# Kernel tuning notes

Measured on AMD Instinct MI355X. Metric: run time of the kernel, lower is better.

Reference implementation:

```python
import jax, jax.numpy as jnp
import numpy as np

B, T, NG, NP = 128, 100, 4096, 512


def setup_inputs() -> dict:
    key = jax.random.key(0)
    ks = jax.random.split(key, 6)
    return {
        "v": jax.random.normal(ks[0], (B, T, 2), dtype=jnp.float32) * 0.1,
        "p0": jax.random.normal(ks[1], (B, NP), dtype=jnp.float32),
        # Linear(Np->Ng, bias=False): weight [Ng, Np]
        "W_enc": jax.random.normal(ks[2], (NG, NP), dtype=jnp.float32) / np.sqrt(NP),
        # nn.RNN weights: W_ih [Ng, 2], W_hh [Ng, Ng], bias=False
        "W_ih": jax.random.normal(ks[3], (NG, 2), dtype=jnp.float32) / np.sqrt(2.0),
        "W_hh": jax.random.normal(ks[4], (NG, NG), dtype=jnp.float32) / np.sqrt(NG),
        # Linear(Ng->Np, bias=True): weight [Np, Ng], bias [Np]
        "W_dec": jax.random.normal(ks[5], (NP, NG), dtype=jnp.float32) / np.sqrt(NG),
        "b_dec": jnp.zeros((NP,), dtype=jnp.float32),
    }


def reference(v, p0, W_enc, W_ih, W_hh, W_dec, b_dec):
    # init hidden state: encoder(p0)  -> [B, Ng]
    h0 = p0 @ W_enc.T
    # precompute input projection for all steps: [T, B, Ng]
    vin = jnp.einsum('bti,gi->tbg', v, W_ih)

    def step(h, x_t):
        h_new = jnp.tanh(x_t + h @ W_hh.T)  # Elman tanh cell, bias=False
        return h_new, h_new

    _, g = jax.lax.scan(step, h0, vin)      # g: [T, B, Ng]
    g = jnp.swapaxes(g, 0, 1)               # [B, T, Ng]
    # decoder: place cell predictions [B, T, Np]
    place_preds = g @ W_dec.T + b_dec
    return place_preds
```

## Files before the change

### kernel.cpp

```cpp
#include <hip/hip_runtime.h>
#include <stdint.h>

namespace {
constexpr int kT = 100;
constexpr int kNG = 4096;
constexpr int kNP = 512;

__device__ __forceinline__ uint16_t f2bf(float f) {
  uint32_t u = __float_as_uint(f);
  u += 0x7FFFu + ((u >> 16) & 1u);
  return (uint16_t)(u >> 16);
}

__device__ __forceinline__ float bfbits(uint32_t lo16) {
  return __uint_as_float(lo16 << 16);
}

__device__ __forceinline__ float fast_tanh(float x) {
  float xc = fminf(fmaxf(x, -15.f), 15.f);
  float e = __expf(2.f * xc);
  return (e - 1.f) / (e + 1.f);
}

__device__ __forceinline__ void gl2lds16(const void* g, void* l) {
  __builtin_amdgcn_global_load_lds((const __attribute__((address_space(1))) unsigned int*)g,
                                   (__attribute__((address_space(3))) unsigned int*)l, 16, 0, 0);
}

__device__ __forceinline__ size_t a_img_off(int b, int g) {
  return ((size_t)(((g >> 7) * 8 + (b >> 4)) * 4 + ((g >> 5) & 3)) * 64 +
          ((g >> 3) & 3) * 16 + (b & 15)) * 8 + (g & 7);
}
}

typedef short bf16x8 __attribute__((ext_vector_type(8)));
typedef float f32x4 __attribute__((ext_vector_type(4)));
typedef uint32_t u32x2 __attribute__((ext_vector_type(2)));

__global__ __launch_bounds__(512) void cvt_whh_kernel(const float* __restrict__ W,
                                                      uint16_t* __restrict__ WhS) {
  const int u = blockIdx.x * 512 + threadIdx.x;
  const int col = u & 15, half = (u >> 4) & 3, ktl = (u >> 6) & 3;
  const int nt = (u >> 8) & 7, chunk = (u >> 11) & 31, gt = u >> 16;
  const int g = gt * 128 + nt * 16 + col;
  const int k0 = chunk * 128 + ktl * 32 + half * 8;
  const float4 x = *(const float4*)(W + (size_t)g * kNG + k0);
  const float4 y = *(const float4*)(W + (size_t)g * kNG + k0 + 4);
  uint4 o;
  o.x = (uint32_t)f2bf(x.x) | ((uint32_t)f2bf(x.y) << 16);
  o.y = (uint32_t)f2bf(x.z) | ((uint32_t)f2bf(x.w) << 16);
  o.z = (uint32_t)f2bf(y.x) | ((uint32_t)f2bf(y.y) << 16);
  o.w = (uint32_t)f2bf(y.z) | ((uint32_t)f2bf(y.w) << 16);
  *(uint4*)(WhS + (size_t)u * 8) = o;
}

__global__ __launch_bounds__(512) void cvt_wdec_kernel(const float* __restrict__ W,
                                                       uint16_t* __restrict__ WdS,
                                                       int* __restrict__ flags) {
  if (blockIdx.x == 511) {
    for (int i = threadIdx.x; i < 2048; i += 512) flags[i] = 0;
  }
  const int u = blockIdx.x * 512 + threadIdx.x;
  const int col = u & 15, half = (u >> 4) & 3, ktl = (u >> 6) & 3;
  const int nt = (u >> 8) & 7, chunk = (u >> 11) & 31, pt = u >> 16;
  const int p = pt * 128 + nt * 16 + col;
  const int k0 = chunk * 128 + ktl * 32 + half * 8;
  const float4 x = *(const float4*)(W + (size_t)p * kNG + k0);
  const float4 y = *(const float4*)(W + (size_t)p * kNG + k0 + 4);
  uint4 o;
  o.x = (uint32_t)f2bf(x.x) | ((uint32_t)f2bf(x.y) << 16);
  o.y = (uint32_t)f2bf(x.z) | ((uint32_t)f2bf(x.w) << 16);
  o.z = (uint32_t)f2bf(y.x) | ((uint32_t)f2bf(y.y) << 16);
  o.w = (uint32_t)f2bf(y.z) | ((uint32_t)f2bf(y.w) << 16);
  *(uint4*)(WdS + (size_t)u * 8) = o;
}

__global__ __launch_bounds__(512, 2) void enc_kernel(const float* __restrict__ p0,
                                                     const float* __restrict__ Wenc,
                                                     uint16_t* __restrict__ H0S) {
  __shared__ alignas(16) uint16_t Wlds[16 * 64 * 8];
  const int tid = threadIdx.x;
  const int g0 = blockIdx.x * 16;
  for (int f = tid; f < 16 * 64; f += 512) {
    const int kt = f >> 6, fl = f & 63;
    const int g = g0 + (fl & 15);
    const int k = kt * 32 + ((fl >> 4) << 3);
    const float* s = Wenc + (size_t)g * kNP + k;
    uint16_t* d = Wlds + f * 8;
#pragma unroll
    for (int j = 0; j < 8; j++) d[j] = f2bf(s[j]);
  }
  __syncthreads();
  const int wave = tid >> 6;
  const int lane = tid & 63;
  const int mrow = wave * 16 + (lane & 15);
  const float* arow = p0 + (size_t)mrow * kNP + ((lane >> 4) << 3);
  f32x4 acc = {0.f, 0.f, 0.f, 0.f};
#pragma unroll
  for (int kt = 0; kt < 16; kt++) {
    const float* ap = arow + kt * 32;
    bf16x8 a;
#pragma unroll
    for (int j = 0; j < 8; j++) a[j] = (short)f2bf(ap[j]);
    bf16x8 b = *(const bf16x8*)(Wlds + (kt * 64 + lane) * 8);
    acc = __builtin_amdgcn_mfma_f32_16x16x32_bf16(a, b, acc, 0, 0, 0);
  }
  const int gcol = g0 + (lane & 15);
  const int rbase = wave * 16 + ((lane >> 4) << 2);
#pragma unroll
  for (int r = 0; r < 4; r++) {
    H0S[a_img_off(rbase + r, gcol)] = f2bf(acc[r]);
  }
}

__global__ __launch_bounds__(512, 2) void rnn_loop_kernel(const float* __restrict__ Whh,
                                                          const uint16_t* __restrict__ H0S,
                                                          uint16_t* __restrict__ Gsw,
                                                          float* __restrict__ Part,
                                                          const float* __restrict__ v,
                                                          const float* __restrict__ Wih,
                                                          int* __restrict__ flags) {
  extern __shared__ uint16_t wlds[];
  const int tid = threadIdx.x;
  const int wave = tid >> 6, lane = tid & 63;
  const int bid = blockIdx.x;
  const int xcd = bid & 7;
  const int gt = xcd * 4 + (bid >> 6);
  const int ks = (bid >> 3) & 7;
  const int mg = wave >> 1, ng = wave & 1;

  int* pcnt = flags;
  int* hcnt = flags + 32 * 32;
  uint16_t* PartB = (uint16_t*)Part;

  {
    const float* wsrc = Whh + (size_t)(gt * 128) * kNG + ks * 512;
#pragma unroll
    for (int i = 0; i < 16; i++) {
      const int u = (i << 9) + tid;
      const int g = u >> 6, ku = u & 63;
      const float* s = wsrc + (size_t)g * kNG + (ku << 3);
      const float4 x = *(const float4*)(s);
      const float4 y = *(const float4*)(s + 4);
      const int lu = (((((ku >> 4) << 3) + (g >> 4)) << 2) + ((ku >> 2) & 3)) * 64 +
                     ((ku & 3) << 4) + (g & 15);
      bf16x8 o;
      o[0] = (short)f2bf(x.x); o[1] = (short)f2bf(x.y);
      o[2] = (short)f2bf(x.z); o[3] = (short)f2bf(x.w);
      o[4] = (short)f2bf(y.x); o[5] = (short)f2bf(y.y);
      o[6] = (short)f2bf(y.z); o[7] = (short)f2bf(y.w);
      *(bf16x8*)(wlds + ((size_t)lu << 3)) = o;
    }
  }
  __syncthreads();

  const int rbred = ks * 16 + (tid >> 5);
  const int gl = (tid & 31) << 2;
  const int gg = gt * 128 + gl;
  uint16_t* myPart = PartB + (((size_t)(gt * 8 + ks)) << 14);

  const float4 w0 = *(const float4*)(Wih + gg * 2);
  const float4 w1 = *(const float4*)(Wih + gg * 2 + 4);

  for (int t = 0; t < kT; t++) {
    if (t > 0) {
      const int target = 8 * t;
      if (tid < 5) {
        int* f = (tid < 4) ? (hcnt + ((ks * 4 + tid) << 5)) : (hcnt + (gt << 5));
        while (__hip_atomic_load(f, __ATOMIC_RELAXED, __HIP_MEMORY_SCOPE_AGENT) < target)
          __builtin_amdgcn_s_sleep(1);
      }
      __builtin_amdgcn_fence(__ATOMIC_ACQUIRE, "workgroup");
      __syncthreads();
    }

    const float v0 = v[(rbred * kT + t) * 2 + 0];
    const float v1 = v[(rbred * kT + t) * 2 + 1];

    const uint16_t* Aimg = (t == 0) ? H0S : (Gsw + (((size_t)(t - 1)) << 19));
    f32x4 acc[2][4];
#pragma unroll
    for (int i = 0; i < 2; i++)
#pragma unroll
      for (int j = 0; j < 4; j++) acc[i][j] = (f32x4){0.f, 0.f, 0.f, 0.f};

#pragma unroll
    for (int kc = 0; kc < 4; kc++) {
      const uint16_t* Ac = Aimg + ((size_t)(ks * 4 + kc) << 14);
      bf16x8 a[2][4];
#pragma unroll
      for (int mi = 0; mi < 2; mi++)
#pragma unroll
        for (int ktl = 0; ktl < 4; ktl++)
          a[mi][ktl] = *(const bf16x8*)(Ac + ((((mg * 2 + mi) * 4 + ktl) * 64 + lane) << 3));
#pragma unroll
      for (int ktl = 0; ktl < 4; ktl++) {
#pragma unroll
        for (int nt = 0; nt < 4; nt++) {
          bf16x8 b = *(const bf16x8*)(wlds + (kc << 14) +
                                      ((((ng * 4 + nt) * 4 + ktl) * 64 + lane) << 3));
          acc[0][nt] = __builtin_amdgcn_mfma_f32_16x16x32_bf16(a[0][ktl], b, acc[0][nt], 0, 0, 0);
          acc[1][nt] = __builtin_amdgcn_mfma_f32_16x16x32_bf16(a[1][ktl], b, acc[1][nt], 0, 0, 0);
        }
      }
    }
    {
      const int gcol0 = (ng << 6);
      const int rbase = (mg << 5) + ((lane >> 4) << 2);
#pragma unroll
      for (int mi = 0; mi < 2; mi++)
#pragma unroll
        for (int nt = 0; nt < 4; nt++)
#pragma unroll
          for (int r = 0; r < 4; r++) {
            const int b = rbase + (mi << 4) + r;
            const int g = gcol0 + (nt << 4) + (lane & 15);
            myPart[(b << 7) + g] = f2bf(acc[mi][nt][r]);
          }
    }
    asm volatile("s_waitcnt vmcnt(0)" ::: "memory");
    __syncthreads();
    if (tid == 0) {
      __hip_atomic_fetch_add(pcnt + (gt << 5), 1, __ATOMIC_RELAXED, __HIP_MEMORY_SCOPE_AGENT);
      const int tgt = 8 * (t + 1);
      while (__hip_atomic_load(pcnt + (gt << 5), __ATOMIC_RELAXED, __HIP_MEMORY_SCOPE_AGENT) < tgt)
        __builtin_amdgcn_s_sleep(1);
      __builtin_amdgcn_fence(__ATOMIC_ACQUIRE, "workgroup");
    }
    __syncthreads();

    {
      const uint16_t* pb = PartB + (((size_t)(gt * 8)) << 14) + (rbred << 7) + gl;
      u32x2 pv[8];
#pragma unroll
      for (int j = 0; j < 8; j++) {
        asm volatile("global_load_dwordx2 %0, %1, off sc0"
                     : "=v"(pv[j])
                     : "v"(pb + ((size_t)j << 14))
                     : "memory");
      }
      asm volatile("s_waitcnt vmcnt(0)" ::: "memory");
      __builtin_amdgcn_sched_barrier(0);
      float s0 = 0.f, s1 = 0.f, s2 = 0.f, s3 = 0.f;
#pragma unroll
      for (int j = 0; j < 8; j++) {
        s0 += bfbits(pv[j][0] & 0xFFFFu);
        s1 += __uint_as_float(pv[j][0] & 0xFFFF0000u);
        s2 += bfbits(pv[j][1] & 0xFFFFu);
        s3 += __uint_as_float(pv[j][1] & 0xFFFF0000u);
      }
      const uint16_t h0 = f2bf(fast_tanh(s0 + v0 * w0.x + v1 * w0.y));
      const uint16_t h1 = f2bf(fast_tanh(s1 + v0 * w0.z + v1 * w0.w));
      const uint16_t h2 = f2bf(fast_tanh(s2 + v0 * w1.x + v1 * w1.y));
      const uint16_t h3 = f2bf(fast_tanh(s3 + v0 * w1.z + v1 * w1.w));
      const uint32_t lo = (uint32_t)h0 | ((uint32_t)h1 << 16);
      const uint32_t hi = (uint32_t)h2 | ((uint32_t)h3 << 16);
      const unsigned long long uval = ((unsigned long long)hi << 32) | lo;
      uint16_t* Gt = Gsw + (((size_t)t) << 19);
      __hip_atomic_exchange((unsigned long long*)(Gt + a_img_off(rbred, gg)), uval,
                            __ATOMIC_RELAXED, __HIP_MEMORY_SCOPE_AGENT);
    }
    asm volatile("s_waitcnt vmcnt(0)" ::: "memory");
    __syncthreads();
    if (tid == 0)
      __hip_atomic_fetch_add(hcnt + (gt << 5), 1, __ATOMIC_RELAXED, __HIP_MEMORY_SCOPE_AGENT);
  }
}

__global__ __launch_bounds__(512, 4) void stepmm_kernel(const uint16_t* __restrict__ Asrc,
                                                        const uint16_t* __restrict__ WhS,
                                                        float* __restrict__ Part) {
  __shared__ alignas(16) uint16_t lds[32768];
  const int tid = threadIdx.x;
  const int wave = tid >> 6, lane = tid & 63;
  const int gt = blockIdx.x >> 3, ks = blockIdx.x & 7;
  const int mg = wave >> 1, ng = wave & 1;
  const uint16_t* Wbase = WhS + ((size_t)gt << 19);
  f32x4 acc[2][4];
#pragma unroll
  for (int i = 0; i < 2; i++)
#pragma unroll
    for (int j = 0; j < 4; j++) acc[i][j] = (f32x4){0.f, 0.f, 0.f, 0.f};

  for (int kc = 0; kc < 4; kc++) {
    const int chunk = ks * 4 + kc;
    const uint16_t* Ac = Asrc + ((size_t)chunk << 14);
    const uint16_t* Bc = Wbase + ((size_t)chunk << 14);
#pragma unroll
    for (int i = 0; i < 8; i++) {
      const int j = wave * 8 + i;
      const uint16_t* s = (j < 32) ? (Ac + (j << 9)) : (Bc + ((j - 32) << 9));
      gl2lds16(s + (lane << 3), (void*)(lds + (j << 9)));
    }
    __syncthreads();
    const uint16_t* lA = lds;
    const uint16_t* lB = lds + 16384;
#pragma unroll
    for (int ktl = 0; ktl < 4; ktl++) {
      bf16x8 a0 = *(const bf16x8*)(lA + ((((mg * 2 + 0) * 4 + ktl) * 64 + lane) << 3));
      bf16x8 a1 = *(const bf16x8*)(lA + ((((mg * 2 + 1) * 4 + ktl) * 64 + lane) << 3));
#pragma unroll
      for (int nt = 0; nt < 4; nt++) {
        bf16x8 b = *(const bf16x8*)(lB + ((((ng * 4 + nt) * 4 + ktl) * 64 + lane) << 3));
        acc[0][nt] = __builtin_amdgcn_mfma_f32_16x16x32_bf16(a0, b, acc[0][nt], 0, 0, 0);
        acc[1][nt] = __builtin_amdgcn_mfma_f32_16x16x32_bf16(a1, b, acc[1][nt], 0, 0, 0);
      }
    }
    __syncthreads();
  }
  const int g0 = (gt << 7) + (ng << 6);
  const int rb = (mg << 5) + ((lane >> 4) << 2);
#pragma unroll
  for (int mi = 0; mi < 2; mi++)
#pragma unroll
    for (int nt = 0; nt < 4; nt++)
#pragma unroll
      for (int r = 0; r < 4; r++) {
        const int b = rb + (mi << 4) + r;
        const int g = g0 + (nt << 4) + (lane & 15);
        Part[(((size_t)(ks * 128 + b)) << 12) + g] = acc[mi][nt][r];
      }
}

__global__ __launch_bounds__(256) void steptanh_kernel(const float* __restrict__ Part,
                                                       const float* __restrict__ v,
                                                       const float* __restrict__ Wih,
                                                       uint16_t* __restrict__ Gt, int t) {
  const int tg = blockIdx.x * 256 + threadIdx.x;
  const int b = tg >> 9;
  const int g0 = (tg & 511) << 3;
  float s[8];
#pragma unroll
  for (int j = 0; j < 8; j++) s[j] = 0.f;
#pragma unroll
  for (int ks = 0; ks < 8; ks++) {
    const float4* p = (const float4*)(Part + (((size_t)(ks * 128 + b)) << 12) + g0);
    const float4 x = p[0], y = p[1];
    s[0] += x.x; s[1] += x.y; s[2] += x.z; s[3] += x.w;
    s[4] += y.x; s[5] += y.y; s[6] += y.z; s[7] += y.w;
  }
  const float v0 = v[(b * kT + t) * 2 + 0];
  const float v1 = v[(b * kT + t) * 2 + 1];
  uint16_t h[8];
#pragma unroll
  for (int j = 0; j < 8; j++) {
    const int g = g0 + j;
    const float pre = s[j] + v0 * Wih[g * 2 + 0] + v1 * Wih[g * 2 + 1];
    h[j] = f2bf(fast_tanh(pre));
  }
  uint4 u;
  u.x = (uint32_t)h[0] | ((uint32_t)h[1] << 16);
  u.y = (uint32_t)h[2] | ((uint32_t)h[3] << 16);
  u.z = (uint32_t)h[4] | ((uint32_t)h[5] << 16);
  u.w = (uint32_t)h[6] | ((uint32_t)h[7] << 16);
  const size_t off = ((size_t)(((g0 >> 7) * 8 + (b >> 4)) * 4 + ((g0 >> 5) & 3)) * 64 +
                      ((g0 >> 3) & 3) * 16 + (b & 15)) * 8;
  *(uint4*)(Gt + off) = u;
}

__global__ __launch_bounds__(512, 4) void dec_kernel(const uint16_t* __restrict__ Gsw,
                                                     const uint16_t* __restrict__ WdS,
                                                     const float* __restrict__ bd,
                                                     float* __restrict__ out) {
  __shared__ alignas(16) uint16_t lds[32768];
  const int slot = blockIdx.x & 7;
  const int m = blockIdx.x >> 3;
  const int t = slot + ((m >> 2) << 3);
  const int pt = m & 3;
  if (t >= kT) return;
  const int tid = threadIdx.x;
  const int wave = tid >> 6, lane = tid & 63;
  const int mg = wave >> 1, ng = wave & 1;
  const uint16_t* Abase = Gsw + (size_t)t * 524288;
  const uint16_t* Bbase = WdS + (size_t)pt * 524288;
  f32x4 acc[2][4];
#pragma unroll
  for (int i = 0; i < 2; i++)
#pragma unroll
    for (int j = 0; j < 4; j++) acc[i][j] = (f32x4){0.f, 0.f, 0.f, 0.f};

  for (int chunk = 0; chunk < 32; chunk++) {
    const uint16_t* Ac = Abase + ((size_t)chunk << 14);
    const uint16_t* Bc = Bbase + ((size_t)chunk << 14);
#pragma unroll
    for (int i = 0; i < 8; i++) {
      const int j = wave * 8 + i;
      const uint16_t* s = (j < 32) ? (Ac + (j << 9)) : (Bc + ((j - 32) << 9));
      gl2lds16(s + (lane << 3), (void*)(lds + (j << 9)));
    }
    __syncthreads();
    const uint16_t* lA = lds;
    const uint16_t* lB = lds + 16384;
#pragma unroll
    for (int ktl = 0; ktl < 4; ktl++) {
      bf16x8 a0 = *(const bf16x8*)(lA + ((((mg * 2 + 0) * 4 + ktl) * 64 + lane) << 3));
      bf16x8 a1 = *(const bf16x8*)(lA + ((((mg * 2 + 1) * 4 + ktl) * 64 + lane) << 3));
#pragma unroll
      for (int nt = 0; nt < 4; nt++) {
        bf16x8 b = *(const bf16x8*)(lB + ((((ng * 4 + nt) * 4 + ktl) * 64 + lane) << 3));
        acc[0][nt] = __builtin_amdgcn_mfma_f32_16x16x32_bf16(a0, b, acc[0][nt], 0, 0, 0);
        acc[1][nt] = __builtin_amdgcn_mfma_f32_16x16x32_bf16(a1, b, acc[1][nt], 0, 0, 0);
      }
    }
    __syncthreads();
  }
  const int p0c = (pt << 7) + (ng << 6);
  const int rb = (mg << 5) + ((lane >> 4) << 2);
#pragma unroll
  for (int mi = 0; mi < 2; mi++)
#pragma unroll
    for (int nt = 0; nt < 4; nt++) {
      const int p = p0c + (nt << 4) + (lane & 15);
      const float bias = bd[p];
#pragma unroll
      for (int r = 0; r < 4; r++) {
        const int b = rb + (mi << 4) + r;
        out[((size_t)b * kT + t) * kNP + p] = acc[mi][nt][r] + bias;
      }
    }
}

extern "C" void kernel_launch(void* const* d_in, const int* in_sizes, int n_in,
                              void* d_out, int out_size, void* d_ws, size_t ws_size,
                              hipStream_t stream) {
  const float* v    = (const float*)d_in[0];
  const float* p0   = (const float*)d_in[1];
  const float* Wenc = (const float*)d_in[2];
  const float* Wih  = (const float*)d_in[3];
  const float* Whh  = (const float*)d_in[4];
  const float* Wdec = (const float*)d_in[5];
  const float* bdec = (const float*)d_in[6];
  float* out = (float*)d_out;

  uint8_t* ws = (uint8_t*)d_ws;
  uint16_t* WhS = (uint16_t*)(ws);
  uint16_t* WdS = (uint16_t*)(ws + 33554432);
  uint16_t* H0S = (uint16_t*)(ws + 37748736);
  uint16_t* Gsw = (uint16_t*)(ws + 38797312);
  float*    Part = (float*)(ws + 143654912);
  int*      flags = (int*)(ws + 160432128);

  cvt_wdec_kernel<<<512, 512, 0, stream>>>(Wdec, WdS, flags);
  enc_kernel<<<256, 512, 0, stream>>>(p0, Wenc, H0S);

  const float* Whh_c = Whh;
  const uint16_t* H0S_c = H0S;
  void* args[7] = {(void*)&Whh_c, (void*)&H0S_c, (void*)&Gsw, (void*)&Part,
                   (void*)&v, (void*)&Wih, (void*)&flags};
  hipError_t e = hipLaunchCooperativeKernel(rnn_loop_kernel, dim3(256), dim3(512), args,
                                            (unsigned int)131072, stream);
  if (e != hipSuccess) {
    (void)hipGetLastError();
    cvt_whh_kernel<<<4096, 512, 0, stream>>>(Whh, WhS);
    for (int t = 0; t < kT; t++) {
      const uint16_t* Asrc = (t == 0) ? H0S : (Gsw + (size_t)(t - 1) * 524288);
      stepmm_kernel<<<256, 512, 0, stream>>>(Asrc, WhS, Part);
      steptanh_kernel<<<256, 256, 0, stream>>>(Part, v, Wih, Gsw + (size_t)t * 524288, t);
    }
  }

  dec_kernel<<<416, 512, 0, stream>>>(Gsw, WdS, bdec, out);
}
```

Before: 1.047 ms.

## Split recurrent matmul K dimension across twice as many cooperative blocks

The persistent RNN kernel now launches 512 blocks instead of 256. Each block handles a 256-wide K slice of W_hh, so it keeps half the weights in LDS (64KB) and does half the MFMA work per step. The cross-block reduction now sums 16 bf16 partials instead of 8, and each thread produces two hidden outputs instead of four. The aim is to shorten the per-step critical path of the latency-bound recurrence. The cost is more partial-sum traffic and more blocks taking part in every flag synchronisation.

```diff
diff --git a/kernel.cpp b/kernel.cpp
--- a/kernel.cpp
+++ b/kernel.cpp
@@ -35,7 +35,6 @@
 
 typedef short bf16x8 __attribute__((ext_vector_type(8)));
 typedef float f32x4 __attribute__((ext_vector_type(4)));
-typedef uint32_t u32x2 __attribute__((ext_vector_type(2)));
 
 __global__ __launch_bounds__(512) void cvt_whh_kernel(const float* __restrict__ W,
                                                       uint16_t* __restrict__ WhS) {
@@ -113,7 +112,7 @@
   }
 }
 
-__global__ __launch_bounds__(512, 2) void rnn_loop_kernel(const float* __restrict__ Whh,
+__global__ __launch_bounds__(512, 4) void rnn_loop_kernel(const float* __restrict__ Whh,
                                                           const uint16_t* __restrict__ H0S,
                                                           uint16_t* __restrict__ Gsw,
                                                           float* __restrict__ Part,
@@ -125,8 +124,8 @@
   const int wave = tid >> 6, lane = tid & 63;
   const int bid = blockIdx.x;
   const int xcd = bid & 7;
-  const int gt = xcd * 4 + (bid >> 6);
-  const int ks = (bid >> 3) & 7;
+  const int gt = xcd * 4 + (bid >> 7);
+  const int ks2 = (bid >> 3) & 15;
   const int mg = wave >> 1, ng = wave & 1;
 
   int* pcnt = flags;
@@ -134,11 +133,11 @@
   uint16_t* PartB = (uint16_t*)Part;
 
   {
-    const float* wsrc = Whh + (size_t)(gt * 128) * kNG + ks * 512;
-#pragma unroll
-    for (int i = 0; i < 16; i++) {
+    const float* wsrc = Whh + (size_t)(gt * 128) * kNG + ks2 * 256;
+#pragma unroll
+    for (int i = 0; i < 8; i++) {
       const int u = (i << 9) + tid;
-      const int g = u >> 6, ku = u & 63;
+      const int g = u >> 5, ku = u & 31;
       const float* s = wsrc + (size_t)g * kNG + (ku << 3);
       const float4 x = *(const float4*)(s);
       const float4 y = *(const float4*)(s + 4);
@@ -154,19 +153,18 @@
   }
   __syncthreads();
 
-  const int rbred = ks * 16 + (tid >> 5);
-  const int gl = (tid & 31) << 2;
+  const int rbred = ks2 * 8 + (tid >> 6);
+  const int gl = (tid & 63) << 1;
   const int gg = gt * 128 + gl;
-  uint16_t* myPart = PartB + (((size_t)(gt * 8 + ks)) << 14);
-
-  const float4 w0 = *(const float4*)(Wih + gg * 2);
-  const float4 w1 = *(const float4*)(Wih + gg * 2 + 4);
+  uint16_t* myPart = PartB + (((size_t)(gt * 16 + ks2)) << 14);
+
+  const float4 w01 = *(const float4*)(Wih + gg * 2);
 
   for (int t = 0; t < kT; t++) {
     if (t > 0) {
-      const int target = 8 * t;
-      if (tid < 5) {
-        int* f = (tid < 4) ? (hcnt + ((ks * 4 + tid) << 5)) : (hcnt + (gt << 5));
+      const int target = 16 * t;
+      if (tid < 3) {
+        int* f = (tid < 2) ? (hcnt + ((ks2 * 2 + tid) << 5)) : (hcnt + (gt << 5));
         while (__hip_atomic_load(f, __ATOMIC_RELAXED, __HIP_MEMORY_SCOPE_AGENT) < target)
           __builtin_amdgcn_s_sleep(1);
       }
@@ -185,8 +183,8 @@
       for (int j = 0; j < 4; j++) acc[i][j] = (f32x4){0.f, 0.f, 0.f, 0.f};
 
 #pragma unroll
-    for (int kc = 0; kc < 4; kc++) {
-      const uint16_t* Ac = Aimg + ((size_t)(ks * 4 + kc) << 14);
+    for (int kc = 0; kc < 2; kc++) {
+      const uint16_t* Ac = Aimg + ((size_t)(ks2 * 2 + kc) << 14);
       bf16x8 a[2][4];
 #pragma unroll
       for (int mi = 0; mi < 2; mi++)
@@ -222,7 +220,7 @@
     __syncthreads();
     if (tid == 0) {
       __hip_atomic_fetch_add(pcnt + (gt << 5), 1, __ATOMIC_RELAXED, __HIP_MEMORY_SCOPE_AGENT);
-      const int tgt = 8 * (t + 1);
+      const int tgt = 16 * (t + 1);
       while (__hip_atomic_load(pcnt + (gt << 5), __ATOMIC_RELAXED, __HIP_MEMORY_SCOPE_AGENT) < tgt)
         __builtin_amdgcn_s_sleep(1);
       __builtin_amdgcn_fence(__ATOMIC_ACQUIRE, "workgroup");
@@ -230,34 +228,28 @@
     __syncthreads();
 
     {
-      const uint16_t* pb = PartB + (((size_t)(gt * 8)) << 14) + (rbred << 7) + gl;
-      u32x2 pv[8];
-#pragma unroll
-      for (int j = 0; j < 8; j++) {
-        asm volatile("global_load_dwordx2 %0, %1, off sc0"
+      const uint16_t* pb = PartB + (((size_t)(gt * 16)) << 14) + (rbred << 7) + gl;
+      uint32_t pv[16];
+#pragma unroll
+      for (int j = 0; j < 16; j++) {
+        asm volatile("global_load_dword %0, %1, off sc0"
                      : "=v"(pv[j])
                      : "v"(pb + ((size_t)j << 14))
                      : "memory");
       }
       asm volatile("s_waitcnt vmcnt(0)" ::: "memory");
       __builtin_amdgcn_sched_barrier(0);
-      float s0 = 0.f, s1 = 0.f, s2 = 0.f, s3 = 0.f;
-#pragma unroll
-      for (int j = 0; j < 8; j++) {
-        s0 += bfbits(pv[j][0] & 0xFFFFu);
-        s1 += __uint_as_float(pv[j][0] & 0xFFFF0000u);
-        s2 += bfbits(pv[j][1] & 0xFFFFu);
-        s3 += __uint_as_float(pv[j][1] & 0xFFFF0000u);
-      }
-      const uint16_t h0 = f2bf(fast_tanh(s0 + v0 * w0.x + v1 * w0.y));
-      const uint16_t h1 = f2bf(fast_tanh(s1 + v0 * w0.z + v1 * w0.w));
-      const uint16_t h2 = f2bf(fast_tanh(s2 + v0 * w1.x + v1 * w1.y));
-      const uint16_t h3 = f2bf(fast_tanh(s3 + v0 * w1.z + v1 * w1.w));
-      const uint32_t lo = (uint32_t)h0 | ((uint32_t)h1 << 16);
-      const uint32_t hi = (uint32_t)h2 | ((uint32_t)h3 << 16);
-      const unsigned long long uval = ((unsigned long long)hi << 32) | lo;
+      float s0 = 0.f, s1 = 0.f;
+#pragma unroll
+      for (int j = 0; j < 16; j++) {
+        s0 += bfbits(pv[j] & 0xFFFFu);
+        s1 += __uint_as_float(pv[j] & 0xFFFF0000u);
+      }
+      const uint16_t h0 = f2bf(fast_tanh(s0 + v0 * w01.x + v1 * w01.y));
+      const uint16_t h1 = f2bf(fast_tanh(s1 + v0 * w01.z + v1 * w01.w));
+      const uint32_t uval = (uint32_t)h0 | ((uint32_t)h1 << 16);
       uint16_t* Gt = Gsw + (((size_t)t) << 19);
-      __hip_atomic_exchange((unsigned long long*)(Gt + a_img_off(rbred, gg)), uval,
+      __hip_atomic_exchange((uint32_t*)(Gt + a_img_off(rbred, gg)), uval,
                             __ATOMIC_RELAXED, __HIP_MEMORY_SCOPE_AGENT);
     }
     asm volatile("s_waitcnt vmcnt(0)" ::: "memory");
@@ -447,8 +439,8 @@
   const uint16_t* H0S_c = H0S;
   void* args[7] = {(void*)&Whh_c, (void*)&H0S_c, (void*)&Gsw, (void*)&Part,
                    (void*)&v, (void*)&Wih, (void*)&flags};
-  hipError_t e = hipLaunchCooperativeKernel(rnn_loop_kernel, dim3(256), dim3(512), args,
-                                            (unsigned int)131072, stream);
+  hipError_t e = hipLaunchCooperativeKernel(rnn_loop_kernel, dim3(512), dim3(512), args,
+                                            (unsigned int)65536, stream);
   if (e != hipSuccess) {
     (void)hipGetLastError();
     cvt_whh_kernel<<<4096, 512, 0, stream>>>(Whh, WhS);
```

Measured after the change: 2.657 ms. +153.7%, slower.
